# Optimization experiments

Hardware: AMD Instinct MI355X
Metric: run time of the kernel (lower is better)

The kernel has to match this reference:

```python
import jax, jax.numpy as jnp
import numpy as np

NTOKEN = 64          # vocabulary size
MAX_PREFIX_LEN = 4   # tree depth D
D_MODEL = 648        # >= NTOKEN*(2*D+2) + D + 1 = 645


def setup_inputs() -> dict:
    key = jax.random.key(0)
    S, B = 2048, 8
    src = jax.random.randint(key, (S, B), 0, NTOKEN, dtype=jnp.int32)
    return {"src": src}


def _forward(src):
    n, D, d_model = NTOKEN, MAX_PREFIX_LEN, D_MODEL
    S, B = src.shape
    f32 = jnp.float32
    # shifted[k][t, b] = src[t-k, b] if t >= k else -1.
    # The -1 sentinel reproduces the all-zero one-hot rows the torch code creates
    # by zeroing extended_one_hot[0:i, :, ntoken*i].
    shifted = [src] + [
        jnp.concatenate([jnp.full((k, B), -1, src.dtype), src[: S - k]], axis=0)
        for k in range(1, D + 1)
    ]
    # one-hot blocks for offsets 0..D (sentinel -1 -> all-zero row)
    tok_ids = jnp.arange(n, dtype=src.dtype)
    onehots = [(s[..., None] == tok_ids).astype(f32) for s in shifted]  # each [S,B,n]
    one_hot0 = onehots[0]

    mask = jnp.tril(jnp.ones((S, S), f32), k=-1)  # mask[q, j] = 1 iff j < q

    # Incremental depth-i prefix match: at depth i the torch code compares
    # j_part block m (offset m+1, row j) against i_part block m (offset m, row q)
    # for m = 0..i-1; one-hot vectors are equal iff both tokens equal or both
    # out-of-range, which the sentinel encoding captures exactly.
    match = jnp.ones((S, S, B), bool)
    avg_blocks, count_chans = [], []
    for i in range(1, D + 1):
        match = match & (shifted[i - 1][:, None, :] == shifted[i][None, :, :])
        masked = match.astype(f32) * mask[:, :, None]            # [S(q), S(j), B]
        sums = jnp.einsum('qjb,jbt->qbt', masked, one_hot0)      # matched next-token one-hot sums
        counts = masked.sum(axis=1)[..., None]                   # [S, B, 1]
        avg_blocks.append(sums / jnp.clip(counts, 1))
        count_chans.append(counts)

    # Unconditional causal average over all j < q (exclusive prefix mean)
    cs = jnp.cumsum(one_hot0, axis=0)
    excl = jnp.concatenate([jnp.zeros((1, B, n), f32), cs[:-1]], axis=0)
    q_counts = jnp.broadcast_to(jnp.arange(S, dtype=f32)[:, None, None], (S, B, 1))
    avg_u = excl / jnp.clip(q_counts, 1)

    used = n * (2 * D + 2) + D + 1
    pad = jnp.zeros((S, B, d_model - used), f32)
    # channel layout (matches torch scatter/slice positions exactly):
    #   [0 .. n*(D+1))           one-hot blocks, offsets 0..D
    #   [n*(D+1) .. n*(2D+1))    depth-i matched averages, i=1..D
    #   [n*(2D+1) .. n*(2D+2))   unconditional causal average
    #   n*(2D+2)+i-1             depth-i match counts, i=1..D
    #   n*(2D+2)+D               unconditional count (= q)
    parts = onehots + avg_blocks + [avg_u] + count_chans + [q_counts, pad]
    return jnp.concatenate(parts, axis=-1)


def reference(src):
    return _forward(src)
```

## Files before the change

kernel.cpp:

```cpp
#include <hip/hip_runtime.h>

typedef unsigned long long u64;
typedef unsigned int u32;
typedef unsigned short u16;
typedef unsigned char u8;

#define S_LEN 2048
#define BATCH 8
#define DMODEL 648
#define NBLK 32


__global__ __launch_bounds__(64) void k1_rows(const int* __restrict__ src,
                                              ulonglong2* __restrict__ PAIR,
                                              u64* __restrict__ PG,
                                              u8* __restrict__ SRC8) {
    const int w = blockIdx.x, b = blockIdx.y;
    const int lane = threadIdx.x;
    const int p = (w << 6) + lane;
    const int tok  = src[p * BATCH + b];
    const int tokp = (w > 0) ? src[(p - 64) * BATCH + b] : -1;
    u64 m_sel = 0, mp_sel = 0;
    #pragma unroll 8
    for (int t = 0; t < 64; ++t) {
        const u64 m  = __ballot(tok == t);
        const u64 mp = __ballot(tokp == t);
        if (lane == t) { m_sel = m; mp_sel = mp; }
    }
    const int idx = b * 2048 + (w << 6) + lane;
    PG[idx] = m_sel;
    ulonglong2 pr;
    pr.x = (m_sel << 1) | (mp_sel >> 63);
    pr.y = (m_sel << 2) | (mp_sel >> 62);
    PAIR[idx] = pr;
    SRC8[b * 2048 + p] = (u8)tok;
}

__global__ __launch_bounds__(256) void k2_tables(const ulonglong2* __restrict__ PAIR,
                                                 const u64* __restrict__ PG,
                                                 u16* __restrict__ PB,
                                                 u16* __restrict__ PU,
                                                 u16* __restrict__ PS1,
                                                 u32* __restrict__ RB) {
    const int b = blockIdx.y;
    const int x = blockIdx.x * 4 + (threadIdx.x >> 6);
    const int lane = threadIdx.x & 63;
    const int base = b * 2048;

    u32 cntPB = 0;
    u32 pu = 0;
    u32 ps1 = 0;
    u32 rb = 0;
    for (int w = 0; w < NBLK; ++w) {
        const int i0 = base + (w << 6);
        const ulonglong2 pr = PAIR[i0 + x];
        const u64 pv  = PG[i0 + lane];
        const u64 s1l = PAIR[i0 + lane].x;
        PB[(size_t)(b * NBLK + w) * 4096 + (x << 6) + lane] = (u16)cntPB;
        cntPB += (u32)__popcll(pr.x & pv);
        if (x == 0) PU[(b * NBLK + w) * 64 + lane] = (u16)pu;
        pu += (u32)__popcll(pv);
        if (lane == 0) PS1[(b * NBLK + w) * 64 + x] = (u16)ps1;
        ps1 += (u32)__popcll(pr.x);
        rb |= ((pr.y & s1l) != 0ull ? 1u : 0u) << w;
    }
    RB[(b << 12) + (x << 6) + lane] = rb;
}

__global__ __launch_bounds__(256, 4) void k3_compute(const ulonglong2* __restrict__ PAIR,
                                                     const u64* __restrict__ PG,
                                                     const u16* __restrict__ PB,
                                                     const u16* __restrict__ PU,
                                                     const u16* __restrict__ PS1,
                                                     const u32* __restrict__ RB,
                                                     const u8* __restrict__ SRC8,
                                                     float* __restrict__ out) {
    __shared__ __align__(16) ulonglong2 Lpair[2048];
    __shared__ u8 Lsrc[2048];

    const int b = blockIdx.y;
    const int tid = threadIdx.x;
    const int lane = tid & 63;
    const int wv = tid >> 6;

    {
        const ulonglong2* G = PAIR + b * 2048;
        for (int i = tid; i < 2048; i += 256) Lpair[i] = G[i];
        ((u64*)Lsrc)[tid] = ((const u64*)(SRC8 + b * 2048))[tid & 255];
    }
    __syncthreads();

    const u64* PGb  = PG + b * 2048;
    const u16* PBb  = PB + (size_t)b * NBLK * 4096;
    const u16* PUb  = PU + b * NBLK * 64;
    const u16* PS1b = PS1 + b * NBLK * 64;
    const u32* RBb  = RB + (b << 12);

    const int uq = blockIdx.x * 4 + wv;
    const int q0 = uq << 2;

    int tk[8];
    #pragma unroll
    for (int i = 0; i < 8; ++i) {
        const int idx = q0 - 4 + i;
        tk[i] = (idx >= 0) ? (int)Lsrc[idx] : 0;
    }

    #pragma unroll
    for (int r = 0; r < 4; ++r) {
        const int q = q0 + r;
        const int t0 = tk[4 + r], t1 = tk[3 + r], t2 = tk[2 + r], t3 = tk[1 + r];
        const int cq = q >> 6, rem = q & 63;
        const int cbase = cq << 6;
        const u64 valid = (1ull << rem) - 1ull;

        const ulonglong2 pa = Lpair[cbase + t0];
        const ulonglong2 pbq = Lpair[cbase + t1];
        const u64 M1p = pa.x & valid;

        int c1 = (int)PS1b[cbase + t0] + __popcll(M1p);
        int h1 = (int)PBb[((size_t)cq << 12) + (t0 << 6) + lane];
        int cu = (int)PUb[cbase + lane];
        const u64 pvq = PGb[cbase + lane];
        cu += __popcll(pvq & valid);

        u64 mrem = M1p;
        while (mrem) {
            const int jj = __builtin_ctzll(mrem);
            mrem &= mrem - 1;
            const int tj = (int)Lsrc[cbase + jj];
            h1 += (lane == tj) ? 1 : 0;
        }

        int c2 = 0, c3 = 0, c4 = 0, h2 = 0, h3 = 0, h4 = 0;
        const u64 M2p = M1p & pbq.y;
        if (M2p) {
            const u64 cS2  = Lpair[cbase + t2].y;
            const u64 cS2p = cq ? Lpair[cbase - 64 + t2].y : 0ull;
            const u64 dS2  = Lpair[cbase + t3].y;
            const u64 dS2p = cq ? Lpair[cbase - 64 + t3].y : 0ull;
            const u64 M3p = M2p & ((cS2 << 1) | (cS2p >> 63));
            const u64 M4p = M3p & ((dS2 << 2) | (dS2p >> 62));
            c2 += __popcll(M2p); h2 += __popcll(M2p & pvq);
            c3 += __popcll(M3p); h3 += __popcll(M3p & pvq);
            c4 += __popcll(M4p); h4 += __popcll(M4p & pvq);
        }
        u32 rare = RBb[(t1 << 6) + t0] & ((1u << cq) - 1u);
        while (rare) {
            const int w = __builtin_ctz(rare);
            rare &= rare - 1;
            const int wb = w << 6;
            const u64 M2 = Lpair[wb + t0].x & Lpair[wb + t1].y;
            const u64 cS2  = Lpair[wb + t2].y;
            const u64 cS2p = w ? Lpair[wb - 64 + t2].y : 0ull;
            const u64 dS2  = Lpair[wb + t3].y;
            const u64 dS2p = w ? Lpair[wb - 64 + t3].y : 0ull;
            const u64 M3 = M2 & ((cS2 << 1) | (cS2p >> 63));
            const u64 M4 = M3 & ((dS2 << 2) | (dS2p >> 62));
            const u64 pvw = PGb[wb + lane];
            c2 += __popcll(M2); h2 += __popcll(M2 & pvw);
            c3 += __popcll(M3); h3 += __popcll(M3 & pvw);
            c4 += __popcll(M4); h4 += __popcll(M4 & pvw);
        }

        float* op = out + ((size_t)q * BATCH + b) * DMODEL;
        #pragma unroll
        for (int m = 0; m <= 4; ++m) {
            const bool sent = (q - m) < 0;
            op[m * 64 + lane] = (!sent && lane == tk[4 + r - m]) ? 1.f : 0.f;
        }
        op[320 + lane] = (float)h1 / (float)(c1 ? c1 : 1);
        op[384 + lane] = (float)h2 / (float)(c2 ? c2 : 1);
        op[448 + lane] = (float)h3 / (float)(c3 ? c3 : 1);
        op[512 + lane] = (float)h4 / (float)(c4 ? c4 : 1);
        op[576 + lane] = (float)cu / (float)(q ? q : 1);
        if (lane < 8) {
            float v = 0.f;
            if (lane == 0) v = (float)c1;
            else if (lane == 1) v = (float)c2;
            else if (lane == 2) v = (float)c3;
            else if (lane == 3) v = (float)c4;
            else if (lane == 4) v = (float)q;
            op[640 + lane] = v;
        }
    }
}

extern "C" void kernel_launch(void* const* d_in, const int* in_sizes, int n_in,
                              void* d_out, int out_size, void* d_ws, size_t ws_size,
                              hipStream_t stream) {
    const int* src = (const int*)d_in[0];
    float* out = (float*)d_out;
    char* ws = (char*)d_ws;
    ulonglong2* PAIR = (ulonglong2*)(ws);
    u64* PG   = (u64*)(ws + (512u << 10));
    u16* PB   = (u16*)(ws + (640u << 10));
    u16* PU   = (u16*)(ws + (2688u << 10));
    u16* PS1  = (u16*)(ws + (2720u << 10));
    u32* RB   = (u32*)(ws + (2752u << 10));
    u8*  SRC8 = (u8*)(ws + (2880u << 10));

    k1_rows<<<dim3(NBLK, BATCH), 64, 0, stream>>>(src, PAIR, PG, SRC8);
    k2_tables<<<dim3(16, BATCH), 256, 0, stream>>>(PAIR, PG, PB, PU, PS1, RB);
    k3_compute<<<dim3(128, BATCH), 256, 0, stream>>>(PAIR, PG, PB, PU, PS1, RB, SRC8, out);
}
```

Before: 85.60 us.

## Fuse table-building kernels and drop LDS staging in compute kernel

Merges the row-bitmask and prefix-table kernels into one kernel that builds token bitmasks via LDS atomicOr and computes the tables from shared memory, removing a launch and a global round trip. Each block recomputes the bitmasks redundantly, and only block 0 writes PAIR/PG/SRC8. The compute kernel no longer stages PAIR in LDS; it handles two rows per wave with loads hoisted and shared between the rows, reads tokens via packed u64 loads, and replaces the depth-1 histogram loop with a popcount against PG. It also changes the workspace layout and doubles the compute grid. The added risk is more scattered global loads in the rare path.

```diff
diff --git a/kernel.cpp b/kernel.cpp
--- a/kernel.cpp
+++ b/kernel.cpp
@@ -11,150 +11,159 @@
 #define NBLK 32
 
 
-__global__ __launch_bounds__(64) void k1_rows(const int* __restrict__ src,
-                                              ulonglong2* __restrict__ PAIR,
-                                              u64* __restrict__ PG,
-                                              u8* __restrict__ SRC8) {
-    const int w = blockIdx.x, b = blockIdx.y;
-    const int lane = threadIdx.x;
-    const int p = (w << 6) + lane;
-    const int tok  = src[p * BATCH + b];
-    const int tokp = (w > 0) ? src[(p - 64) * BATCH + b] : -1;
-    u64 m_sel = 0, mp_sel = 0;
-    #pragma unroll 8
-    for (int t = 0; t < 64; ++t) {
-        const u64 m  = __ballot(tok == t);
-        const u64 mp = __ballot(tokp == t);
-        if (lane == t) { m_sel = m; mp_sel = mp; }
-    }
-    const int idx = b * 2048 + (w << 6) + lane;
-    PG[idx] = m_sel;
-    ulonglong2 pr;
-    pr.x = (m_sel << 1) | (mp_sel >> 63);
-    pr.y = (m_sel << 2) | (mp_sel >> 62);
-    PAIR[idx] = pr;
-    SRC8[b * 2048 + p] = (u8)tok;
-}
-
-__global__ __launch_bounds__(256) void k2_tables(const ulonglong2* __restrict__ PAIR,
-                                                 const u64* __restrict__ PG,
+__global__ __launch_bounds__(256) void k12_build(const int* __restrict__ src,
+                                                 ulonglong2* __restrict__ PAIR,
+                                                 u64* __restrict__ PG,
                                                  u16* __restrict__ PB,
                                                  u16* __restrict__ PU,
                                                  u16* __restrict__ PS1,
-                                                 u32* __restrict__ RB) {
+                                                 u32* __restrict__ RB,
+                                                 u8* __restrict__ SRC8) {
+    __shared__ __align__(16) ulonglong2 Lpair[2048];
+    __shared__ u64 LP[2048];
+
+    const int b = blockIdx.y, gx = blockIdx.x;
+    const int tid = threadIdx.x, lane = tid & 63, wv = tid >> 6;
+
+    int myt[8];
+    #pragma unroll
+    for (int k = 0; k < 8; ++k) {
+        const int i = tid + 256 * k;
+        myt[k] = src[i * BATCH + b];
+        LP[i] = 0;
+    }
+    __syncthreads();
+    #pragma unroll
+    for (int k = 0; k < 8; ++k) {
+        const int i = tid + 256 * k;
+        atomicOr(&LP[(i & ~63) | myt[k]], 1ull << (i & 63));
+    }
+    __syncthreads();
+    #pragma unroll
+    for (int k = 0; k < 8; ++k) {
+        const int i = tid + 256 * k;
+        const u64 m = LP[i];
+        const u64 mp = (i >= 64) ? LP[i - 64] : 0ull;
+        ulonglong2 pr;
+        pr.x = (m << 1) | (mp >> 63);
+        pr.y = (m << 2) | (mp >> 62);
+        Lpair[i] = pr;
+        if (gx == 0) {
+            PG[b * 2048 + i] = m;
+            PAIR[b * 2048 + i] = pr;
+            SRC8[b * 2048 + i] = (u8)myt[k];
+        }
+    }
+    __syncthreads();
+
+    #pragma unroll 1
+    for (int j = 0; j < 2; ++j) {
+        const int x = gx * 8 + wv * 2 + j;
+        u32 cnt = 0, ps1 = 0, rb = 0, pu = 0;
+        for (int w = 0; w < NBLK; ++w) {
+            const int wb = w << 6;
+            const ulonglong2 prx = Lpair[wb + x];
+            const u64 pvl = LP[wb + lane];
+            const u64 s1l = Lpair[wb + lane].x;
+            PB[(size_t)(b * NBLK + w) * 4096 + (x << 6) + lane] = (u16)cnt;
+            cnt += (u32)__popcll(prx.x & pvl);
+            if (x == 0) { PU[(b * NBLK + w) * 64 + lane] = (u16)pu; pu += (u32)__popcll(pvl); }
+            if (lane == 0) PS1[(b * NBLK + w) * 64 + x] = (u16)ps1;
+            ps1 += (u32)__popcll(prx.x);
+            rb |= ((prx.y & s1l) != 0ull ? 1u : 0u) << w;
+        }
+        RB[(b << 12) + (x << 6) + lane] = rb;
+    }
+}
+
+__global__ __launch_bounds__(256) void k3_compute(const ulonglong2* __restrict__ PAIR,
+                                                  const u64* __restrict__ PG,
+                                                  const u16* __restrict__ PB,
+                                                  const u16* __restrict__ PU,
+                                                  const u16* __restrict__ PS1,
+                                                  const u32* __restrict__ RB,
+                                                  const u8* __restrict__ SRC8,
+                                                  float* __restrict__ out) {
     const int b = blockIdx.y;
-    const int x = blockIdx.x * 4 + (threadIdx.x >> 6);
-    const int lane = threadIdx.x & 63;
-    const int base = b * 2048;
-
-    u32 cntPB = 0;
-    u32 pu = 0;
-    u32 ps1 = 0;
-    u32 rb = 0;
-    for (int w = 0; w < NBLK; ++w) {
-        const int i0 = base + (w << 6);
-        const ulonglong2 pr = PAIR[i0 + x];
-        const u64 pv  = PG[i0 + lane];
-        const u64 s1l = PAIR[i0 + lane].x;
-        PB[(size_t)(b * NBLK + w) * 4096 + (x << 6) + lane] = (u16)cntPB;
-        cntPB += (u32)__popcll(pr.x & pv);
-        if (x == 0) PU[(b * NBLK + w) * 64 + lane] = (u16)pu;
-        pu += (u32)__popcll(pv);
-        if (lane == 0) PS1[(b * NBLK + w) * 64 + x] = (u16)ps1;
-        ps1 += (u32)__popcll(pr.x);
-        rb |= ((pr.y & s1l) != 0ull ? 1u : 0u) << w;
-    }
-    RB[(b << 12) + (x << 6) + lane] = rb;
-}
-
-__global__ __launch_bounds__(256, 4) void k3_compute(const ulonglong2* __restrict__ PAIR,
-                                                     const u64* __restrict__ PG,
-                                                     const u16* __restrict__ PB,
-                                                     const u16* __restrict__ PU,
-                                                     const u16* __restrict__ PS1,
-                                                     const u32* __restrict__ RB,
-                                                     const u8* __restrict__ SRC8,
-                                                     float* __restrict__ out) {
-    __shared__ __align__(16) ulonglong2 Lpair[2048];
-    __shared__ u8 Lsrc[2048];
-
-    const int b = blockIdx.y;
-    const int tid = threadIdx.x;
-    const int lane = tid & 63;
-    const int wv = tid >> 6;
-
-    {
-        const ulonglong2* G = PAIR + b * 2048;
-        for (int i = tid; i < 2048; i += 256) Lpair[i] = G[i];
-        ((u64*)Lsrc)[tid] = ((const u64*)(SRC8 + b * 2048))[tid & 255];
-    }
-    __syncthreads();
-
+    const int tid = threadIdx.x, lane = tid & 63, wv = tid >> 6;
+    const int u = blockIdx.x * 4 + wv;
+    const int q0 = u << 1;
+
+    const ulonglong2* PAb = PAIR + b * 2048;
     const u64* PGb  = PG + b * 2048;
     const u16* PBb  = PB + (size_t)b * NBLK * 4096;
-    const u16* PUb  = PU + b * NBLK * 64;
-    const u16* PS1b = PS1 + b * NBLK * 64;
+    const u16* PUb  = PU + b * 2048;
+    const u16* PS1b = PS1 + b * 2048;
     const u32* RBb  = RB + (b << 12);
 
-    const int uq = blockIdx.x * 4 + wv;
-    const int q0 = uq << 2;
-
-    int tk[8];
-    #pragma unroll
-    for (int i = 0; i < 8; ++i) {
+    const int base = (q0 >= 4) ? (q0 - 4) : 0;
+    const u64* sp = (const u64*)(SRC8 + b * 2048 + (base & ~7));
+    const u64 lo = sp[0], hi = sp[1];
+    const int o = (base & 7) * 8;
+    const u64 tb = o ? ((lo >> o) | (hi << (64 - o))) : lo;
+    int tk[6];
+    #pragma unroll
+    for (int i = 0; i < 6; ++i) {
         const int idx = q0 - 4 + i;
-        tk[i] = (idx >= 0) ? (int)Lsrc[idx] : 0;
-    }
-
-    #pragma unroll
-    for (int r = 0; r < 4; ++r) {
+        const int bix = idx - base;
+        const int sh = (bix > 0 ? bix : 0) * 8;
+        tk[i] = (idx >= 0) ? (int)((tb >> sh) & 0xFF) : 0;
+    }
+
+    const int cq = q0 >> 6, rem0 = q0 & 63;
+    const int cbase = cq << 6;
+    const u64 v0 = (1ull << rem0) - 1ull;
+    const u64 v1 = (2ull << rem0) - 1ull;
+
+    const u64 pvq = PGb[cbase + lane];
+    const int puq = (int)PUb[cbase + lane];
+    const ulonglong2 A = PAb[cbase + tk[4]];
+    const u64 B1 = PAb[cbase + tk[5]].x;
+    const u64 C2 = ((const u64*)&PAb[cbase + tk[3]])[1];
+    const int ps1_[2] = {(int)PS1b[cbase + tk[4]], (int)PS1b[cbase + tk[5]]};
+    const int hb_[2]  = {(int)PBb[((size_t)cq << 12) + (tk[4] << 6) + lane],
+                         (int)PBb[((size_t)cq << 12) + (tk[5] << 6) + lane]};
+    const u32 rbm = (1u << cq) - 1u;
+    const u32 rare_[2] = {RBb[(tk[3] << 6) + tk[4]] & rbm,
+                          RBb[(tk[4] << 6) + tk[5]] & rbm};
+    const u64 M1row_[2] = {A.x, B1};
+    const u64 S2row_[2] = {C2, A.y};
+    const u64 vv_[2] = {v0, v1};
+
+    #pragma unroll
+    for (int r = 0; r < 2; ++r) {
         const int q = q0 + r;
         const int t0 = tk[4 + r], t1 = tk[3 + r], t2 = tk[2 + r], t3 = tk[1 + r];
-        const int cq = q >> 6, rem = q & 63;
-        const int cbase = cq << 6;
-        const u64 valid = (1ull << rem) - 1ull;
-
-        const ulonglong2 pa = Lpair[cbase + t0];
-        const ulonglong2 pbq = Lpair[cbase + t1];
-        const u64 M1p = pa.x & valid;
-
-        int c1 = (int)PS1b[cbase + t0] + __popcll(M1p);
-        int h1 = (int)PBb[((size_t)cq << 12) + (t0 << 6) + lane];
-        int cu = (int)PUb[cbase + lane];
-        const u64 pvq = PGb[cbase + lane];
-        cu += __popcll(pvq & valid);
-
-        u64 mrem = M1p;
-        while (mrem) {
-            const int jj = __builtin_ctzll(mrem);
-            mrem &= mrem - 1;
-            const int tj = (int)Lsrc[cbase + jj];
-            h1 += (lane == tj) ? 1 : 0;
-        }
+        const u64 valid = vv_[r];
+
+        const u64 M1p = M1row_[r] & valid;
+        int c1 = ps1_[r] + __popcll(M1p);
+        int h1 = hb_[r] + __popcll(M1p & pvq);
+        int cu = puq + __popcll(pvq & valid);
 
         int c2 = 0, c3 = 0, c4 = 0, h2 = 0, h3 = 0, h4 = 0;
-        const u64 M2p = M1p & pbq.y;
+        const u64 M2p = M1p & S2row_[r];
         if (M2p) {
-            const u64 cS2  = Lpair[cbase + t2].y;
-            const u64 cS2p = cq ? Lpair[cbase - 64 + t2].y : 0ull;
-            const u64 dS2  = Lpair[cbase + t3].y;
-            const u64 dS2p = cq ? Lpair[cbase - 64 + t3].y : 0ull;
+            const u64 cS2  = ((const u64*)&PAb[cbase + t2])[1];
+            const u64 cS2p = cq ? ((const u64*)&PAb[cbase - 64 + t2])[1] : 0ull;
+            const u64 dS2  = ((const u64*)&PAb[cbase + t3])[1];
+            const u64 dS2p = cq ? ((const u64*)&PAb[cbase - 64 + t3])[1] : 0ull;
             const u64 M3p = M2p & ((cS2 << 1) | (cS2p >> 63));
             const u64 M4p = M3p & ((dS2 << 2) | (dS2p >> 62));
             c2 += __popcll(M2p); h2 += __popcll(M2p & pvq);
             c3 += __popcll(M3p); h3 += __popcll(M3p & pvq);
             c4 += __popcll(M4p); h4 += __popcll(M4p & pvq);
         }
-        u32 rare = RBb[(t1 << 6) + t0] & ((1u << cq) - 1u);
+        u32 rare = rare_[r];
         while (rare) {
             const int w = __builtin_ctz(rare);
             rare &= rare - 1;
             const int wb = w << 6;
-            const u64 M2 = Lpair[wb + t0].x & Lpair[wb + t1].y;
-            const u64 cS2  = Lpair[wb + t2].y;
-            const u64 cS2p = w ? Lpair[wb - 64 + t2].y : 0ull;
-            const u64 dS2  = Lpair[wb + t3].y;
-            const u64 dS2p = w ? Lpair[wb - 64 + t3].y : 0ull;
+            const u64 M2 = PAb[wb + t0].x & ((const u64*)&PAb[wb + t1])[1];
+            const u64 cS2  = ((const u64*)&PAb[wb + t2])[1];
+            const u64 cS2p = w ? ((const u64*)&PAb[wb - 64 + t2])[1] : 0ull;
+            const u64 dS2  = ((const u64*)&PAb[wb + t3])[1];
+            const u64 dS2p = w ? ((const u64*)&PAb[wb - 64 + t3])[1] : 0ull;
             const u64 M3 = M2 & ((cS2 << 1) | (cS2p >> 63));
             const u64 M4 = M3 & ((dS2 << 2) | (dS2p >> 62));
             const u64 pvw = PGb[wb + lane];
@@ -193,14 +202,13 @@
     float* out = (float*)d_out;
     char* ws = (char*)d_ws;
     ulonglong2* PAIR = (ulonglong2*)(ws);
-    u64* PG   = (u64*)(ws + (512u << 10));
-    u16* PB   = (u16*)(ws + (640u << 10));
-    u16* PU   = (u16*)(ws + (2688u << 10));
-    u16* PS1  = (u16*)(ws + (2720u << 10));
-    u32* RB   = (u32*)(ws + (2752u << 10));
-    u8*  SRC8 = (u8*)(ws + (2880u << 10));
-
-    k1_rows<<<dim3(NBLK, BATCH), 64, 0, stream>>>(src, PAIR, PG, SRC8);
-    k2_tables<<<dim3(16, BATCH), 256, 0, stream>>>(PAIR, PG, PB, PU, PS1, RB);
-    k3_compute<<<dim3(128, BATCH), 256, 0, stream>>>(PAIR, PG, PB, PU, PS1, RB, SRC8, out);
+    u64* PG   = (u64*)(ws + (256u << 10));
+    u16* PB   = (u16*)(ws + (384u << 10));
+    u16* PU   = (u16*)(ws + (2432u << 10));
+    u16* PS1  = (u16*)(ws + (2464u << 10));
+    u32* RB   = (u32*)(ws + (2496u << 10));
+    u8*  SRC8 = (u8*)(ws + (2624u << 10));
+
+    k12_build<<<dim3(8, BATCH), 256, 0, stream>>>(src, PAIR, PG, PB, PU, PS1, RB, SRC8);
+    k3_compute<<<dim3(256, BATCH), 256, 0, stream>>>(PAIR, PG, PB, PU, PS1, RB, SRC8, out);
 }
```

Result: faster. 81.64 us (-4.6%).
